# Performance work log

Measured on AMD Instinct MI355X. Metric: run time of the kernel, lower is better.

Reference implementation:

```python
import jax, jax.numpy as jnp
import numpy as np

NUM_PROJS = 8
BLOCK = 128      # key_block_size; with n=4096 -> 32 blocks, query_block_size=128 too
SAMPLE = 128     # sample_size
HEAD_DIM = 64
SCALE = HEAD_DIM ** -0.5

def _gray_perm(n):
    # AngularLSH._unit_hamming_distance_array: Gray-code ordering of 2^n sign buckets
    a = np.array([0, 1], dtype=np.int32)
    for _ in range(n - 1):
        a = np.concatenate([a, a[::-1] + a.shape[0]])
    return a

PERM = jnp.asarray(_gray_perm(NUM_PROJS))
ENC = jnp.asarray(2 ** np.arange(NUM_PROJS), dtype=jnp.int32)

def _lsh_hash(x, proj_dir):
    # x: [b,h,n,d], proj_dir: [d,r] -> Gray-coded bucket id [b,h,n]
    bits = (jnp.einsum('bhnd,dr->bhnr', x, proj_dir) > 0).astype(jnp.int32)
    return PERM[jnp.sum(bits * ENC, axis=-1)]

def _gather_seq(x, idx):
    # gather along seq axis (axis=2); idx: [b,h,m]
    return jnp.take_along_axis(x, idx[..., None], axis=2)

def _hyper_attention(q, k, v, proj_dir, sampled_set):
    # q,k,v: [b,h,n,d]; non-causal HyperAttention (n >= min_seq_len path)
    b, h, n, d = q.shape
    # --- 1. sortLSH block-diagonal attention ---
    q_idx = jnp.argsort(_lsh_hash(q, proj_dir), axis=2, stable=True)
    k_idx = jnp.argsort(_lsh_hash(k, proj_dir), axis=2, stable=True)
    q_idx_inv = jnp.argsort(q_idx, axis=2, stable=True)
    qs = _gather_seq(q, q_idx)
    ks = _gather_seq(k, k_idx)
    vs = _gather_seq(v, k_idx)
    nb = n // BLOCK
    qb = qs.reshape(b, h, nb, BLOCK, d)
    kb = ks.reshape(b, h, nb, BLOCK, d)
    vb = vs.reshape(b, h, nb, BLOCK, d)
    s = jnp.einsum('bhgqd,bhgkd->bhgqk', qb, kb) * SCALE
    lse_blk = jax.scipy.special.logsumexp(s, axis=-1).reshape(b, h, n)
    attn_blk = jnp.einsum('bhgqk,bhgkd->bhgqd', jax.nn.softmax(s, axis=-1), vb).reshape(b, h, n, d)
    # --- 2. uniformly sampled residual (low-rank correction) ---
    ksub = _gather_seq(ks, sampled_set)   # [b,h,m,d]
    vsub = _gather_seq(vs, sampled_set)
    row_blk = jnp.arange(n) // BLOCK       # query_block_size == BLOCK here
    mask = row_blk[None, None, :, None] == (sampled_set // BLOCK)[:, :, None, :]
    bias = jnp.where(mask, jnp.finfo(q.dtype).min, jnp.zeros((), q.dtype))
    sr = jnp.einsum('bhnd,bhmd->bhnm', qs, ksub) * SCALE + bias
    lse_res = jax.scipy.special.logsumexp(sr, axis=-1) + jnp.log(jnp.asarray(n / SAMPLE, q.dtype))
    attn_res = jnp.einsum('bhnm,bhmd->bhnd', jax.nn.softmax(sr, axis=-1), vsub)
    # --- combine the two attention estimates (add_self_attentions) ---
    lse = jnp.logaddexp(lse_blk, lse_res)
    w1 = jnp.exp(lse_blk - lse)[..., None]
    attn = w1 * attn_blk + (1.0 - w1) * attn_res
    # --- unsort rows back to original query order ---
    return _gather_seq(attn, q_idx_inv)

def setup_inputs() -> dict:
    key = jax.random.key(0)
    k1, k2, k3 = jax.random.split(key, 3)
    qkv = jax.random.normal(k1, (2, 4096, 3, 16, 64), dtype=jnp.float32)
    proj_dir = jax.random.normal(k2, (64, NUM_PROJS), dtype=jnp.float32)
    sampled_set = jax.random.randint(k3, (2, 16, SAMPLE), 0, 4096)
    return {"qkv": qkv, "proj_dir": proj_dir, "sampled_set": sampled_set}

def reference(qkv, proj_dir, sampled_set):
    # qkv: [B,S,3,H,D] -> q,k,v [B,H,S,D]
    q = jnp.transpose(qkv[:, :, 0], (0, 2, 1, 3))
    k = jnp.transpose(qkv[:, :, 1], (0, 2, 1, 3))
    v = jnp.transpose(qkv[:, :, 2], (0, 2, 1, 3))
    out = _hyper_attention(q, k, v, proj_dir, sampled_set)
    return jnp.transpose(out, (0, 2, 1, 3))  # [B,S,H,D]
```

## Files before the change

### kernel.cpp

```cpp
#include <hip/hip_runtime.h>
#include <hip/hip_bf16.h>

#define NSEQ 4096
#define NBH 32
#define LOG32 3.4657359028f
#define QSCALE 0.125f

typedef unsigned short us8 __attribute__((ext_vector_type(8)));
typedef __bf16 bf16x8 __attribute__((ext_vector_type(8)));
typedef float f32x4 __attribute__((ext_vector_type(4)));
typedef unsigned int u32x4 __attribute__((ext_vector_type(4)));

__device__ __forceinline__ unsigned short f2b(float x) {
    __bf16 h = (__bf16)x;
    return __builtin_bit_cast(unsigned short, h);
}
__device__ __forceinline__ unsigned pk2(float lo, float hi) {
    return (unsigned)f2b(lo) | ((unsigned)f2b(hi) << 16);
}
__device__ __forceinline__ bf16x8 cvt8(float4 a, float4 b) {
    us8 u;
    u[0] = f2b(a.x); u[1] = f2b(a.y); u[2] = f2b(a.z); u[3] = f2b(a.w);
    u[4] = f2b(b.x); u[5] = f2b(b.y); u[6] = f2b(b.z); u[7] = f2b(b.w);
    return __builtin_bit_cast(bf16x8, u);
}

__global__ __launch_bounds__(256) void hash_kernel(const float* __restrict__ qkv,
                                                   const float* __restrict__ proj,
                                                   unsigned short* __restrict__ hsh) {
    __shared__ float pdT[512];
    int tid = threadIdx.x;
    for (int j = tid; j < 512; j += 256) pdT[j] = proj[(j & 63) * 8 + (j >> 6)];
    __syncthreads();
    int j0 = blockIdx.x * 256 + tid;
    #pragma unroll
    for (int rep = 0; rep < 2; ++rep) {
        int j = j0 + rep * 131072;
        int ch = rep;
        int bh = (j >> 12) & 31;
        int i = j & 4095;
        int b = bh >> 4, h = bh & 15;
        const float4* src = (const float4*)(qkv + ((size_t)((b * NSEQ + i) * 3 + ch)) * 1024 + h * 64);
        double acc[8] = {0, 0, 0, 0, 0, 0, 0, 0};
        for (int d4 = 0; d4 < 16; ++d4) {
            float4 x = src[d4];
            double xx = x.x, xy = x.y, xz = x.z, xw = x.w;
            #pragma unroll
            for (int r = 0; r < 8; ++r) {
                const float4 p = *(const float4*)&pdT[r * 64 + d4 * 4];
                acc[r] += xx * p.x + xy * p.y + xz * p.z + xw * p.w;
            }
        }
        int c = 0;
        #pragma unroll
        for (int r = 0; r < 8; ++r)
            if (acc[r] > 0.0) c |= (1 << r);
        hsh[j] = (unsigned short)(c ^ (c >> 1));
    }
}

__global__ __launch_bounds__(1024) void sort_kernel(const unsigned short* __restrict__ hsh,
                                                    int* __restrict__ qidx,
                                                    int* __restrict__ kidx) {
    int blk = blockIdx.x;
    int pass = blk >> 5, bh = blk & 31;
    const unsigned short* src = hsh + pass * 131072 + bh * 4096;
    int* outg = (pass ? kidx : qidx) + bh * 4096;
    int tid = threadIdx.x;
    __shared__ unsigned short hl[4096];
    __shared__ int hist[64][256];
    __shared__ int base[256];
    for (int j = tid; j < 64 * 256; j += 1024) (&hist[0][0])[j] = 0;
    __syncthreads();
    for (int j = tid; j < 4096; j += 1024) {
        unsigned short v = src[j];
        hl[j] = v;
        atomicAdd(&hist[j >> 6][v], 1);
    }
    __syncthreads();
    int cnt_tot = 0;
    if (tid < 256) {
        int tot = 0;
        #pragma unroll
        for (int s = 0; s < 64; ++s) { int c = hist[s][tid]; hist[s][tid] = tot; tot += c; }
        base[tid] = tot;
        cnt_tot = tot;
    }
    __syncthreads();
    for (int off = 1; off < 256; off <<= 1) {
        int t = (tid >= off && tid < 256) ? base[tid - off] : 0;
        __syncthreads();
        if (tid >= off && tid < 256) base[tid] += t;
        __syncthreads();
    }
    int incl = 0;
    if (tid < 256) incl = base[tid];
    __syncthreads();
    if (tid < 256) base[tid] = incl - cnt_tot;
    __syncthreads();
    {
        int seg = tid >> 4, cls = tid & 15;
        for (int ii = 0; ii < 64; ++ii) {
            int i = (seg << 6) + ii;
            int q = hl[i];
            if ((q & 15) == cls) {
                int pos = base[q] + hist[seg][q];
                hist[seg][q] = hist[seg][q] + 1;
                outg[pos] = i;
            }
        }
    }
}

__global__ __launch_bounds__(512, 4) void attn_kernel(const float* __restrict__ qkv,
                                                      const int* __restrict__ sampled,
                                                      const int* __restrict__ qidx_g,
                                                      const int* __restrict__ kidx_g,
                                                      float* __restrict__ out) {
    int gb = blockIdx.x;
    int bh = gb >> 5, g = gb & 31;
    int b = bh >> 4, h = bh & 15;
    int tid = threadIdx.x;
    int w = tid >> 6, l = tid & 63;
    int l15 = l & 15, lq = l >> 4;

    __shared__ us8 KP[2048];
    __shared__ us8 VT[2048];
    __shared__ float colbias[256];
    __shared__ int qrow[128];
    __shared__ int krow[256];

    if (tid < 128) {
        qrow[tid] = qidx_g[bh * NSEQ + g * 128 + tid];
        krow[tid] = kidx_g[bh * NSEQ + g * 128 + tid];
        colbias[tid] = 0.0f;
    } else if (tid < 256) {
        int j = tid - 128;
        int sp = sampled[bh * 128 + j];
        krow[tid] = kidx_g[bh * NSEQ + sp];
        colbias[tid] = ((sp >> 7) == g) ? -1e30f : LOG32;
    }
    __syncthreads();

    int qr = qrow[w * 16 + l15];
    const float* qbase = qkv + ((size_t)((b * NSEQ + qr) * 3 + 0)) * 1024 + h * 64 + lq * 8;
    float4 qa0 = *(const float4*)(qbase);
    float4 qa1 = *(const float4*)(qbase + 4);
    float4 qb0 = *(const float4*)(qbase + 32);
    float4 qb1 = *(const float4*)(qbase + 36);

    #pragma unroll
    for (int rep = 0; rep < 2; ++rep) {
        int job = tid + rep * 512;
        int r = job >> 2, qt = job & 3;
        const float4* src = (const float4*)(qkv + ((size_t)((b * NSEQ + krow[r]) * 3 + 1)) * 1024 + h * 64 + qt * 16);
        float4 f0 = src[0], f1 = src[1], f2 = src[2], f3 = src[3];
        int sw = (r ^ (r >> 2)) & 7;
        KP[r * 8 + ((qt * 2) ^ sw)] = __builtin_bit_cast(us8, cvt8(f0, f1));
        KP[r * 8 + ((qt * 2 + 1) ^ sw)] = __builtin_bit_cast(us8, cvt8(f2, f3));
    }
    {
        int key = tid >> 1, half = tid & 1;
        const float4* src = (const float4*)(qkv + ((size_t)((b * NSEQ + krow[key]) * 3 + 2)) * 1024 + h * 64 + half * 32);
        unsigned short* vt_us = (unsigned short*)VT;
        int kc8 = key >> 3, ke = key & 7;
        #pragma unroll
        for (int d4 = 0; d4 < 8; ++d4) {
            float4 f = src[d4];
            int d = half * 32 + d4 * 4;
            vt_us[(((d + 0) * 32 + (kc8 ^ ((d + 0) & 7))) << 3) + ke] = f2b(f.x);
            vt_us[(((d + 1) * 32 + (kc8 ^ ((d + 1) & 7))) << 3) + ke] = f2b(f.y);
            vt_us[(((d + 2) * 32 + (kc8 ^ ((d + 2) & 7))) << 3) + ke] = f2b(f.z);
            vt_us[(((d + 3) * 32 + (kc8 ^ ((d + 3) & 7))) << 3) + ke] = f2b(f.w);
        }
    }
    __syncthreads();

    bf16x8 q0 = cvt8(qa0, qa1);
    bf16x8 q1 = cvt8(qb0, qb1);
    f32x4 sA[8], sB[8];
    int ra = 8 * (l15 >> 2) + (l15 & 3);
    #pragma unroll
    for (int s = 0; s < 8; ++s) {
        int krA = s * 32 + ra;
        int krB = krA + 4;
        int swA = (krA ^ (krA >> 2)) & 7;
        int swB = (krB ^ (krB >> 2)) & 7;
        bf16x8 kA0 = __builtin_bit_cast(bf16x8, KP[krA * 8 + (lq ^ swA)]);
        bf16x8 kA1 = __builtin_bit_cast(bf16x8, KP[krA * 8 + ((lq + 4) ^ swA)]);
        bf16x8 kB0 = __builtin_bit_cast(bf16x8, KP[krB * 8 + (lq ^ swB)]);
        bf16x8 kB1 = __builtin_bit_cast(bf16x8, KP[krB * 8 + ((lq + 4) ^ swB)]);
        f32x4 accA = {0.f, 0.f, 0.f, 0.f}, accB = {0.f, 0.f, 0.f, 0.f};
        accA = __builtin_amdgcn_mfma_f32_16x16x32_bf16(kA0, q0, accA, 0, 0, 0);
        accA = __builtin_amdgcn_mfma_f32_16x16x32_bf16(kA1, q1, accA, 0, 0, 0);
        accB = __builtin_amdgcn_mfma_f32_16x16x32_bf16(kB0, q0, accB, 0, 0, 0);
        accB = __builtin_amdgcn_mfma_f32_16x16x32_bf16(kB1, q1, accB, 0, 0, 0);
        float4 cbA = *(const float4*)&colbias[s * 32 + lq * 8];
        float4 cbB = *(const float4*)&colbias[s * 32 + lq * 8 + 4];
        sA[s][0] = accA[0] * QSCALE + cbA.x;
        sA[s][1] = accA[1] * QSCALE + cbA.y;
        sA[s][2] = accA[2] * QSCALE + cbA.z;
        sA[s][3] = accA[3] * QSCALE + cbA.w;
        sB[s][0] = accB[0] * QSCALE + cbB.x;
        sB[s][1] = accB[1] * QSCALE + cbB.y;
        sB[s][2] = accB[2] * QSCALE + cbB.z;
        sB[s][3] = accB[3] * QSCALE + cbB.w;
    }

    float m = -1e30f;
    #pragma unroll
    for (int s = 0; s < 8; ++s)
        #pragma unroll
        for (int j = 0; j < 4; ++j) {
            m = fmaxf(m, sA[s][j]);
            m = fmaxf(m, sB[s][j]);
        }
    m = fmaxf(m, __shfl_xor(m, 16));
    m = fmaxf(m, __shfl_xor(m, 32));
    float sum = 0.f;
    #pragma unroll
    for (int s = 0; s < 8; ++s)
        #pragma unroll
        for (int j = 0; j < 4; ++j) {
            float pa = __expf(sA[s][j] - m); sA[s][j] = pa; sum += pa;
            float pb = __expf(sB[s][j] - m); sB[s][j] = pb; sum += pb;
        }
    sum += __shfl_xor(sum, 16);
    sum += __shfl_xor(sum, 32);
    float rs = 1.0f / sum;

    f32x4 oacc[4] = {{0.f,0.f,0.f,0.f},{0.f,0.f,0.f,0.f},{0.f,0.f,0.f,0.f},{0.f,0.f,0.f,0.f}};
    #pragma unroll
    for (int s = 0; s < 8; ++s) {
        u32x4 pw;
        pw[0] = pk2(sA[s][0] * rs, sA[s][1] * rs);
        pw[1] = pk2(sA[s][2] * rs, sA[s][3] * rs);
        pw[2] = pk2(sB[s][0] * rs, sB[s][1] * rs);
        pw[3] = pk2(sB[s][2] * rs, sB[s][3] * rs);
        bf16x8 pa = __builtin_bit_cast(bf16x8, pw);
        #pragma unroll
        for (int ct = 0; ct < 4; ++ct) {
            int d = ct * 16 + l15;
            bf16x8 vb = __builtin_bit_cast(bf16x8, VT[d * 32 + ((s * 4 + lq) ^ (d & 7))]);
            oacc[ct] = __builtin_amdgcn_mfma_f32_16x16x32_bf16(pa, vb, oacc[ct], 0, 0, 0);
        }
    }

    #pragma unroll
    for (int j = 0; j < 4; ++j) {
        int row = w * 16 + lq * 4 + j;
        size_t obase = ((size_t)((b * NSEQ + qrow[row]) * 16 + h)) * 64;
        #pragma unroll
        for (int ct = 0; ct < 4; ++ct)
            out[obase + ct * 16 + l15] = oacc[ct][j];
    }
}

extern "C" void kernel_launch(void* const* d_in, const int* in_sizes, int n_in,
                              void* d_out, int out_size, void* d_ws, size_t ws_size,
                              hipStream_t stream) {
    const float* qkv = (const float*)d_in[0];
    const float* proj = (const float*)d_in[1];
    const int* sampled = (const int*)d_in[2];
    float* outp = (float*)d_out;

    int* qidx = (int*)d_ws;
    int* kidx = qidx + NBH * NSEQ;
    unsigned short* hsh = (unsigned short*)(kidx + NBH * NSEQ);

    hash_kernel<<<512, 256, 0, stream>>>(qkv, proj, hsh);
    sort_kernel<<<64, 1024, 0, stream>>>(hsh, qidx, kidx);
    attn_kernel<<<NBH * 32, 512, 0, stream>>>(qkv, sampled, qidx, kidx, outp);
}
```

Measured before the change: 75.77 us.

## Prefetch V into registers early and defer V transpose after softmax

The V rows are now loaded into registers before the K staging. They are written transposed into LDS only after the QK^T and softmax phase, so their global-load latency overlaps the score computation. The K loads for both row halves are issued together before the LDS stores, and __syncthreads is replaced by an explicit lgkmcnt wait plus s_barrier. This costs more live registers (32 floats held across the softmax) and adds one extra barrier, which may reduce occupancy.

```diff
diff --git a/kernel.cpp b/kernel.cpp
--- a/kernel.cpp
+++ b/kernel.cpp
@@ -23,6 +23,10 @@
     u[0] = f2b(a.x); u[1] = f2b(a.y); u[2] = f2b(a.z); u[3] = f2b(a.w);
     u[4] = f2b(b.x); u[5] = f2b(b.y); u[6] = f2b(b.z); u[7] = f2b(b.w);
     return __builtin_bit_cast(bf16x8, u);
+}
+__device__ __forceinline__ void lds_barrier() {
+    asm volatile("s_waitcnt lgkmcnt(0)" ::: "memory");
+    __builtin_amdgcn_s_barrier();
 }
 
 __global__ __launch_bounds__(256) void hash_kernel(const float* __restrict__ qkv,
@@ -140,7 +144,7 @@
         krow[tid] = kidx_g[bh * NSEQ + sp];
         colbias[tid] = ((sp >> 7) == g) ? -1e30f : LOG32;
     }
-    __syncthreads();
+    lds_barrier();
 
     int qr = qrow[w * 16 + l15];
     const float* qbase = qkv + ((size_t)((b * NSEQ + qr) * 3 + 0)) * 1024 + h * 64 + lq * 8;
@@ -149,32 +153,26 @@
     float4 qb0 = *(const float4*)(qbase + 32);
     float4 qb1 = *(const float4*)(qbase + 36);
 
-    #pragma unroll
-    for (int rep = 0; rep < 2; ++rep) {
-        int job = tid + rep * 512;
-        int r = job >> 2, qt = job & 3;
-        const float4* src = (const float4*)(qkv + ((size_t)((b * NSEQ + krow[r]) * 3 + 1)) * 1024 + h * 64 + qt * 16);
-        float4 f0 = src[0], f1 = src[1], f2 = src[2], f3 = src[3];
-        int sw = (r ^ (r >> 2)) & 7;
-        KP[r * 8 + ((qt * 2) ^ sw)] = __builtin_bit_cast(us8, cvt8(f0, f1));
-        KP[r * 8 + ((qt * 2 + 1) ^ sw)] = __builtin_bit_cast(us8, cvt8(f2, f3));
-    }
+    int vkey = tid >> 1, vhalf = tid & 1;
+    const float4* vsrc = (const float4*)(qkv + ((size_t)((b * NSEQ + krow[vkey]) * 3 + 2)) * 1024 + h * 64 + vhalf * 32);
+    float4 vv0 = vsrc[0], vv1 = vsrc[1], vv2 = vsrc[2], vv3 = vsrc[3];
+    float4 vv4 = vsrc[4], vv5 = vsrc[5], vv6 = vsrc[6], vv7 = vsrc[7];
+
     {
-        int key = tid >> 1, half = tid & 1;
-        const float4* src = (const float4*)(qkv + ((size_t)((b * NSEQ + krow[key]) * 3 + 2)) * 1024 + h * 64 + half * 32);
-        unsigned short* vt_us = (unsigned short*)VT;
-        int kc8 = key >> 3, ke = key & 7;
-        #pragma unroll
-        for (int d4 = 0; d4 < 8; ++d4) {
-            float4 f = src[d4];
-            int d = half * 32 + d4 * 4;
-            vt_us[(((d + 0) * 32 + (kc8 ^ ((d + 0) & 7))) << 3) + ke] = f2b(f.x);
-            vt_us[(((d + 1) * 32 + (kc8 ^ ((d + 1) & 7))) << 3) + ke] = f2b(f.y);
-            vt_us[(((d + 2) * 32 + (kc8 ^ ((d + 2) & 7))) << 3) + ke] = f2b(f.z);
-            vt_us[(((d + 3) * 32 + (kc8 ^ ((d + 3) & 7))) << 3) + ke] = f2b(f.w);
-        }
-    }
-    __syncthreads();
+        int r0 = tid >> 2, qt = tid & 3;
+        int r1 = r0 + 128;
+        const float4* src0 = (const float4*)(qkv + ((size_t)((b * NSEQ + krow[r0]) * 3 + 1)) * 1024 + h * 64 + qt * 16);
+        const float4* src1 = (const float4*)(qkv + ((size_t)((b * NSEQ + krow[r1]) * 3 + 1)) * 1024 + h * 64 + qt * 16);
+        float4 k0 = src0[0], k1 = src0[1], k2 = src0[2], k3 = src0[3];
+        float4 k4 = src1[0], k5 = src1[1], k6 = src1[2], k7 = src1[3];
+        int sw0 = (r0 ^ (r0 >> 2)) & 7;
+        int sw1 = (r1 ^ (r1 >> 2)) & 7;
+        KP[r0 * 8 + ((qt * 2) ^ sw0)]     = __builtin_bit_cast(us8, cvt8(k0, k1));
+        KP[r0 * 8 + ((qt * 2 + 1) ^ sw0)] = __builtin_bit_cast(us8, cvt8(k2, k3));
+        KP[r1 * 8 + ((qt * 2) ^ sw1)]     = __builtin_bit_cast(us8, cvt8(k4, k5));
+        KP[r1 * 8 + ((qt * 2 + 1) ^ sw1)] = __builtin_bit_cast(us8, cvt8(k6, k7));
+    }
+    lds_barrier();
 
     bf16x8 q0 = cvt8(qa0, qa1);
     bf16x8 q1 = cvt8(qb0, qb1);
@@ -229,6 +227,22 @@
     sum += __shfl_xor(sum, 32);
     float rs = 1.0f / sum;
 
+    {
+        unsigned short* vt_us = (unsigned short*)VT;
+        int kc8 = vkey >> 3, ke = vkey & 7;
+        float4 vvs[8] = {vv0, vv1, vv2, vv3, vv4, vv5, vv6, vv7};
+        #pragma unroll
+        for (int d4 = 0; d4 < 8; ++d4) {
+            float4 f = vvs[d4];
+            int d = vhalf * 32 + d4 * 4;
+            vt_us[(((d + 0) * 32 + (kc8 ^ ((d + 0) & 7))) << 3) + ke] = f2b(f.x);
+            vt_us[(((d + 1) * 32 + (kc8 ^ ((d + 1) & 7))) << 3) + ke] = f2b(f.y);
+            vt_us[(((d + 2) * 32 + (kc8 ^ ((d + 2) & 7))) << 3) + ke] = f2b(f.z);
+            vt_us[(((d + 3) * 32 + (kc8 ^ ((d + 3) & 7))) << 3) + ke] = f2b(f.w);
+        }
+    }
+    lds_barrier();
+
     f32x4 oacc[4] = {{0.f,0.f,0.f,0.f},{0.f,0.f,0.f,0.f},{0.f,0.f,0.f,0.f},{0.f,0.f,0.f,0.f}};
     #pragma unroll
     for (int s = 0; s < 8; ++s) {
```

Result: slower. 86.15 us (+13.7%).
